# Kernel tuning notes

Hardware: AMD Instinct MI355X
Metric: run time of the kernel (lower is better)

## Reference

```python
import jax, jax.numpy as jnp
import numpy as np

NEG_SLOPE = 0.2  # PyG GATConv default negative_slope
EPS = 1e-16     # PyG softmax denominator epsilon


def gat_conv(x, src, dst, W, a_src, a_dst, bias):
    """PyG GATConv (concat=True, dropout off). x:[N,Fin], src/dst:[E]."""
    N = x.shape[0]
    H, C = a_src.shape
    h = (x @ W).reshape(N, H, C)                      # per-head projected features
    es = jnp.einsum('nhc,hc->nh', h, a_src)           # alpha_src per node/head
    ed = jnp.einsum('nhc,hc->nh', h, a_dst)           # alpha_dst per node/head
    e = jax.nn.leaky_relu(es[src] + ed[dst], NEG_SLOPE)   # [E,H] edge scores
    # segment softmax over destination nodes (every node has a self loop)
    m = jax.ops.segment_max(e, dst, num_segments=N)
    p = jnp.exp(e - m[dst])
    denom = jax.ops.segment_sum(p, dst, num_segments=N)
    alpha = p / (denom[dst] + EPS)                    # [E,H]
    out = jax.ops.segment_sum(h[src] * alpha[:, :, None], dst, num_segments=N)
    return out.reshape(N, H * C) + bias


def _single_graph(x, ei, W1, a_src1, a_dst1, b1, W2, a_src2, a_dst2, b2):
    N = x.shape[0]
    loop = jnp.arange(N, dtype=ei.dtype)              # add_self_loops=True
    src = jnp.concatenate([ei[0], loop])
    dst = jnp.concatenate([ei[1], loop])
    h = jax.nn.relu(gat_conv(x, src, dst, W1, a_src1, a_dst1, b1))
    # F.dropout with p=0.0 is identity
    return gat_conv(h, src, dst, W2, a_src2, a_dst2, b2)


def setup_inputs() -> dict:
    key = jax.random.key(0)
    ks = jax.random.split(key, 9)
    B, N, E, F_in, H, C = 2, 20000, 320000, 128, 8, 64

    def glorot(k, shape):
        fan_in, fan_out = shape[-2] if len(shape) > 1 else shape[-1], shape[-1]
        s = np.sqrt(6.0 / (fan_in + fan_out)).astype(np.float32)
        return jax.random.uniform(k, shape, jnp.float32, -s, s)

    return {
        'xs': jax.random.normal(ks[0], (B, N, F_in), jnp.float32),
        'edge_indexs': jax.random.randint(ks[1], (B, 2, E), 0, N, jnp.int32),
        'W1': glorot(ks[2], (F_in, H * C)),
        'a_src1': glorot(ks[3], (H, C)),
        'a_dst1': glorot(ks[4], (H, C)),
        'b1': jnp.zeros((H * C,), jnp.float32),
        'W2': glorot(ks[5], (H * C, C)),
        'a_src2': glorot(ks[6], (1, C)),
        'a_dst2': glorot(ks[7], (1, C)),
        'b2': jnp.zeros((C,), jnp.float32),
    }


def reference(xs, edge_indexs, W1, a_src1, a_dst1, b1, W2, a_src2, a_dst2, b2):
    f = lambda x, ei: _single_graph(x, ei, W1, a_src1, a_dst1, b1, W2, a_src2, a_dst2, b2)
    return jax.vmap(f)(xs, edge_indexs)               # [B, N, C]
```

## Files before the change

kernel.cpp:

```cpp
#include <hip/hip_runtime.h>
#include <hip/hip_bf16.h>
#include <cstdint>

#define NEG_SLOPE 0.2f
#define SOFTMAX_EPS 1e-16f
#define NN 20000
#define EE 320000
#define CAP 48

typedef __hip_bfloat16 bf16;
typedef unsigned short ushort;
typedef short s8v __attribute__((ext_vector_type(8)));
typedef float f4v __attribute__((ext_vector_type(4)));
typedef float f2v __attribute__((ext_vector_type(2)));

static __device__ __forceinline__ float lo16(unsigned u) { return __uint_as_float(u << 16); }
static __device__ __forceinline__ float hi16(unsigned u) { return __uint_as_float(u & 0xffff0000u); }
static __device__ __forceinline__ ushort f2bf(float v) {
    bf16 h = __float2bfloat16(v);
    return *(ushort*)&h;
}

__global__ void prep_kernel(const float* __restrict__ W1, const float* __restrict__ W2,
                            ushort* __restrict__ w1hi, ushort* __restrict__ w1lo,
                            ushort* __restrict__ w2hi, ushort* __restrict__ w2lo,
                            int* __restrict__ count) {
    int bid = blockIdx.x;
    int t = threadIdx.x;
    if (bid >= 48) {
        int idx = (bid - 48) * 256 + t;
        if (idx < 2 * NN) count[idx] = 0;
        return;
    }
    __shared__ float T[32][65];
    const float* src; ushort *dhi, *dlo; int K, C, c0, k0;
    if (bid < 32) { src = W1; dhi = w1hi; dlo = w1lo; K = 128; C = 512; c0 = (bid & 7) * 64; k0 = (bid >> 3) * 32; }
    else          { src = W2; dhi = w2hi; dlo = w2lo; K = 512; C = 64;  c0 = 0;              k0 = (bid - 32) * 32; }
    for (int i = 0; i < 8; ++i) {
        int flat = t + i * 256;
        int k = flat >> 6, c = flat & 63;
        T[k][c] = src[(size_t)(k0 + k) * C + c0 + c];
    }
    __syncthreads();
    int c = t >> 2, j0 = (t & 3) * 8;
    unsigned hp[4], lp[4];
#pragma unroll
    for (int p = 0; p < 4; ++p) {
        float v0 = T[j0 + p * 2][c], v1 = T[j0 + p * 2 + 1][c];
        ushort h0 = f2bf(v0), h1 = f2bf(v1);
        float l0 = v0 - __uint_as_float((unsigned)h0 << 16);
        float l1 = v1 - __uint_as_float((unsigned)h1 << 16);
        hp[p] = (unsigned)h0 | ((unsigned)h1 << 16);
        lp[p] = (unsigned)f2bf(l0) | ((unsigned)f2bf(l1) << 16);
    }
    size_t o = (size_t)(c0 + c) * K + k0 + j0;
    *(uint4*)&dhi[o] = make_uint4(hp[0], hp[1], hp[2], hp[3]);
    *(uint4*)&dlo[o] = make_uint4(lp[0], lp[1], lp[2], lp[3]);
}

#define G1S 40
#define GEMM1_BLOCKS 1252
__global__ __launch_bounds__(256) void gemm1_scatter(
        const float* __restrict__ xs, const ushort* __restrict__ w1hi,
        const ushort* __restrict__ w1lo, const float* __restrict__ a_src,
        const float* __restrict__ a_dst, bf16* __restrict__ h1,
        float* __restrict__ es, float* __restrict__ ed,
        const int* __restrict__ ei, int* __restrict__ count,
        ushort* __restrict__ esrc) {
    __shared__ ushort lds[25600];
    int t = threadIdx.x;
    int bid = blockIdx.x;

    if (bid >= GEMM1_BLOCKS) {
        int idx = bid - GEMM1_BLOCKS;
        int b = idx / 1250;
        int e = (idx % 1250) * 256 + t;
        const int* srcA = ei + (size_t)b * 2 * EE;
        int s = srcA[e], d = srcA[EE + e];
        if ((unsigned)d >= NN || (unsigned)s >= NN) return;
        int pos = atomicAdd(&count[b * NN + d], 1);
        if (pos < CAP)
            esrc[((size_t)b * NN + d) * CAP + pos] = (ushort)s;
        return;
    }

    ushort* Xhi = lds;
    ushort* Xlo = lds + 2560;
    ushort* Whi = lds + 5120;
    ushort* Wlo = lds + 15360;
    int w = t >> 6, lane = t & 63, quad = lane >> 4, l16 = lane & 15;
    int b = bid / 626;
    int rem = bid % 626;
    int nhalf = rem / 313;
    int row0 = (rem % 313) * 64, nbase = nhalf * 256;
    const float* x = xs + (size_t)b * NN * 128;
    bf16*  h1b = h1 + (size_t)b * NN * 512;
    float* esb = es + (size_t)b * NN * 8;
    float* edb = ed + (size_t)b * NN * 8;

    f4v acc[16];
#pragma unroll
    for (int i = 0; i < 16; ++i) acc[i] = (f4v)0.f;

    for (int kc = 0; kc < 4; ++kc) {
        __syncthreads();
        {
            int row = t >> 2, c0 = (t & 3) * 8;
            float v[8];
            if (row0 + row < NN) {
                float4 A = *(const float4*)&x[(size_t)(row0 + row) * 128 + kc * 32 + c0];
                float4 B = *(const float4*)&x[(size_t)(row0 + row) * 128 + kc * 32 + c0 + 4];
                v[0] = A.x; v[1] = A.y; v[2] = A.z; v[3] = A.w;
                v[4] = B.x; v[5] = B.y; v[6] = B.z; v[7] = B.w;
            } else {
#pragma unroll
                for (int i = 0; i < 8; ++i) v[i] = 0.f;
            }
            unsigned hp[4], lp[4];
#pragma unroll
            for (int p = 0; p < 4; ++p) {
                ushort h0 = f2bf(v[p * 2]), h1_ = f2bf(v[p * 2 + 1]);
                float l0 = v[p * 2] - __uint_as_float((unsigned)h0 << 16);
                float l1 = v[p * 2 + 1] - __uint_as_float((unsigned)h1_ << 16);
                hp[p] = (unsigned)h0 | ((unsigned)h1_ << 16);
                lp[p] = (unsigned)f2bf(l0) | ((unsigned)f2bf(l1) << 16);
            }
            *(uint4*)&Xhi[row * G1S + c0] = make_uint4(hp[0], hp[1], hp[2], hp[3]);
            *(uint4*)&Xlo[row * G1S + c0] = make_uint4(lp[0], lp[1], lp[2], lp[3]);
        }
        {
            const ushort* sh = w1hi + (size_t)(nbase + t) * 128 + kc * 32;
            const ushort* sl = w1lo + (size_t)(nbase + t) * 128 + kc * 32;
            uint4 h0 = *(const uint4*)(sh), h1_ = *(const uint4*)(sh + 8);
            uint4 h2 = *(const uint4*)(sh + 16), h3 = *(const uint4*)(sh + 24);
            uint4 l0 = *(const uint4*)(sl), l1 = *(const uint4*)(sl + 8);
            uint4 l2 = *(const uint4*)(sl + 16), l3 = *(const uint4*)(sl + 24);
            *(uint4*)&Whi[t * G1S]      = h0; *(uint4*)&Whi[t * G1S + 8]  = h1_;
            *(uint4*)&Whi[t * G1S + 16] = h2; *(uint4*)&Whi[t * G1S + 24] = h3;
            *(uint4*)&Wlo[t * G1S]      = l0; *(uint4*)&Wlo[t * G1S + 8]  = l1;
            *(uint4*)&Wlo[t * G1S + 16] = l2; *(uint4*)&Wlo[t * G1S + 24] = l3;
        }
        __syncthreads();
        int arow = (w * 16 + l16) * G1S + quad * 8;
        s8v ahi = *(const s8v*)&Xhi[arow];
        s8v alo = *(const s8v*)&Xlo[arow];
#pragma unroll
        for (int ct = 0; ct < 16; ++ct) {
            int baddr = (ct * 16 + l16) * G1S + quad * 8;
            s8v bhi = *(const s8v*)&Whi[baddr];
            s8v blo = *(const s8v*)&Wlo[baddr];
            acc[ct] = __builtin_amdgcn_mfma_f32_16x16x32_bf16(ahi, bhi, acc[ct], 0, 0, 0);
            acc[ct] = __builtin_amdgcn_mfma_f32_16x16x32_bf16(ahi, blo, acc[ct], 0, 0, 0);
            acc[ct] = __builtin_amdgcn_mfma_f32_16x16x32_bf16(alo, bhi, acc[ct], 0, 0, 0);
        }
    }

#pragma unroll
    for (int hh = 0; hh < 4; ++hh) {
        float s4[4] = {0.f, 0.f, 0.f, 0.f}, d4[4] = {0.f, 0.f, 0.f, 0.f};
#pragma unroll
        for (int ct4 = 0; ct4 < 4; ++ct4) {
            int ct = hh * 4 + ct4;
            int c = nbase + ct * 16 + l16;
            float as = a_src[c], ad = a_dst[c];
#pragma unroll
            for (int r = 0; r < 4; ++r) { s4[r] += acc[ct][r] * as; d4[r] += acc[ct][r] * ad; }
        }
#pragma unroll
        for (int o = 1; o < 16; o <<= 1) {
#pragma unroll
            for (int r = 0; r < 4; ++r) {
                s4[r] += __shfl_xor(s4[r], o);
                d4[r] += __shfl_xor(d4[r], o);
            }
        }
        if (l16 == 0) {
            int head = nhalf * 4 + hh;
#pragma unroll
            for (int r = 0; r < 4; ++r) {
                int gr = row0 + w * 16 + quad * 4 + r;
                if (gr < NN) { esb[gr * 8 + head] = s4[r]; edb[gr * 8 + head] = d4[r]; }
            }
        }
    }

    __syncthreads();
    ushort* rp = lds + w * 4224;
#pragma unroll
    for (int ct = 0; ct < 16; ++ct)
#pragma unroll
        for (int r = 0; r < 4; ++r)
            rp[(quad * 4 + r) * 264 + ct * 16 + l16] = f2bf(acc[ct][r]);
#pragma unroll
    for (int i = 0; i < 8; ++i) {
        int idx = i * 512 + lane * 8;
        int row = idx >> 8, col = idx & 255;
        uint4 vv = *(const uint4*)&rp[row * 264 + col];
        int gr = row0 + w * 16 + row;
        if (gr < NN) *(uint4*)&h1b[(size_t)gr * 512 + nbase + col] = vv;
    }
}

#define G2S 72
__global__ __launch_bounds__(256) void gemm2_mfma(
        const bf16* __restrict__ a, const ushort* __restrict__ w2hi,
        const ushort* __restrict__ w2lo, const float* __restrict__ a_src,
        const float* __restrict__ a_dst, bf16* __restrict__ h2,
        float* __restrict__ es, float* __restrict__ ed) {
    __shared__ ushort lds[13824];
    ushort* AS  = lds;
    ushort* Whi = lds + 4608;
    ushort* Wlo = lds + 9216;

    int t = threadIdx.x;
    int w = t >> 6, lane = t & 63, quad = lane >> 4, l16 = lane & 15;
    int b = blockIdx.y;
    int row0 = blockIdx.x * 64;
    const bf16* ab = a + (size_t)b * NN * 512;
    bf16*  h2b = h2 + (size_t)b * NN * 64;
    float* esb = es + (size_t)b * NN;
    float* edb = ed + (size_t)b * NN;

    f4v acc[4];
#pragma unroll
    for (int i = 0; i < 4; ++i) acc[i] = (f4v)0.f;

    for (int kc = 0; kc < 8; ++kc) {
        __syncthreads();
        {
            int row = t >> 2, k0 = (t & 3) * 16;
            uint4 q0, q1;
            if (row0 + row < NN) {
                q0 = *(const uint4*)(ab + (size_t)(row0 + row) * 512 + kc * 64 + k0);
                q1 = *(const uint4*)(ab + (size_t)(row0 + row) * 512 + kc * 64 + k0 + 8);
            } else { q0 = make_uint4(0, 0, 0, 0); q1 = q0; }
            *(uint4*)&AS[row * G2S + k0]     = q0;
            *(uint4*)&AS[row * G2S + k0 + 8] = q1;
            const ushort* sh = w2hi + (size_t)row * 512 + kc * 64 + k0;
            const ushort* sl = w2lo + (size_t)row * 512 + kc * 64 + k0;
            *(uint4*)&Whi[row * G2S + k0]     = *(const uint4*)(sh);
            *(uint4*)&Whi[row * G2S + k0 + 8] = *(const uint4*)(sh + 8);
            *(uint4*)&Wlo[row * G2S + k0]     = *(const uint4*)(sl);
            *(uint4*)&Wlo[row * G2S + k0 + 8] = *(const uint4*)(sl + 8);
        }
        __syncthreads();
#pragma unroll
        for (int ks = 0; ks < 2; ++ks) {
            s8v av = *(const s8v*)&AS[(w * 16 + l16) * G2S + ks * 32 + quad * 8];
#pragma unroll
            for (int ct = 0; ct < 4; ++ct) {
                int baddr = (ct * 16 + l16) * G2S + ks * 32 + quad * 8;
                s8v bhi = *(const s8v*)&Whi[baddr];
                s8v blo = *(const s8v*)&Wlo[baddr];
                acc[ct] = __builtin_amdgcn_mfma_f32_16x16x32_bf16(av, bhi, acc[ct], 0, 0, 0);
                acc[ct] = __builtin_amdgcn_mfma_f32_16x16x32_bf16(av, blo, acc[ct], 0, 0, 0);
            }
        }
    }

    {
        float s4[4] = {0.f, 0.f, 0.f, 0.f}, d4[4] = {0.f, 0.f, 0.f, 0.f};
#pragma unroll
        for (int ct = 0; ct < 4; ++ct) {
            int c = ct * 16 + l16;
            float as = a_src[c], ad = a_dst[c];
#pragma unroll
            for (int r = 0; r < 4; ++r) { s4[r] += acc[ct][r] * as; d4[r] += acc[ct][r] * ad; }
        }
#pragma unroll
        for (int o = 1; o < 16; o <<= 1) {
#pragma unroll
            for (int r = 0; r < 4; ++r) {
                s4[r] += __shfl_xor(s4[r], o);
                d4[r] += __shfl_xor(d4[r], o);
            }
        }
        if (l16 == 0) {
#pragma unroll
            for (int r = 0; r < 4; ++r) {
                int gr = row0 + w * 16 + quad * 4 + r;
                if (gr < NN) { esb[gr] = s4[r]; edb[gr] = d4[r]; }
            }
        }
    }

    __syncthreads();
    ushort* rp = lds + w * 1152;
#pragma unroll
    for (int ct = 0; ct < 4; ++ct)
#pragma unroll
        for (int r = 0; r < 4; ++r)
            rp[(quad * 4 + r) * G2S + ct * 16 + l16] = f2bf(acc[ct][r]);
#pragma unroll
    for (int i = 0; i < 2; ++i) {
        int idx = i * 512 + lane * 8;
        int row = idx >> 6, col = idx & 63;
        uint4 vv = *(const uint4*)&rp[row * G2S + col];
        int gr = row0 + w * 16 + row;
        if (gr < NN) *(uint4*)&h2b[(size_t)gr * 64 + col] = vv;
    }
}

__global__ __launch_bounds__(256) void aggregate1_kernel(
        const bf16* __restrict__ h1, const float* __restrict__ es,
        const float* __restrict__ ed, const int* __restrict__ count,
        const ushort* __restrict__ esrc, const float* __restrict__ b1,
        bf16* __restrict__ out1) {
    __shared__ float alds[4][8][60];
    __shared__ unsigned offs[4][60];
    int b = blockIdx.y;
    const bf16*  h1b = h1 + (size_t)b * NN * 512;
    const float* esb = es + (size_t)b * NN * 8;
    const float* edb = ed + (size_t)b * NN * 8;
    bf16* out1b = out1 + (size_t)b * NN * 512;

    int t = threadIdx.x;
    int wv = t >> 6, lane = t & 63;
    int n = blockIdx.x * 4 + wv;
    int deg_e = count[b * NN + n];
    deg_e = max(0, min(deg_e, CAP));
    int deg = deg_e + 1;
    size_t beg = ((size_t)b * NN + n) * CAP;

    float4 ed0 = *(const float4*)&edb[n * 8];
    float4 ed1 = *(const float4*)&edb[n * 8 + 4];
    float edh[8] = {ed0.x, ed0.y, ed0.z, ed0.w, ed1.x, ed1.y, ed1.z, ed1.w};

    bool act = lane < deg;
    int sreg = act ? ((lane < deg_e) ? (int)esrc[beg + lane] : n) : 0;
    const char* eb = (const char*)esb;
    unsigned eoff = (unsigned)sreg << 5;
    float4 s0 = *(const float4*)(eb + eoff);
    float4 s1 = *(const float4*)(eb + eoff + 16);
    float e[8] = {s0.x, s0.y, s0.z, s0.w, s1.x, s1.y, s1.z, s1.w};
    float m[8], p[8], sum[8];
#pragma unroll
    for (int h = 0; h < 8; ++h) {
        float v = e[h] + edh[h];
        v = (v >= 0.f) ? v : NEG_SLOPE * v;
        e[h] = act ? v : -1e30f;
        m[h] = e[h];
    }
#pragma unroll
    for (int o = 32; o > 0; o >>= 1) {
#pragma unroll
        for (int h = 0; h < 8; ++h) m[h] = fmaxf(m[h], __shfl_xor(m[h], o));
    }
#pragma unroll
    for (int h = 0; h < 8; ++h) { p[h] = act ? __expf(e[h] - m[h]) : 0.f; sum[h] = p[h]; }
#pragma unroll
    for (int o = 32; o > 0; o >>= 1) {
#pragma unroll
        for (int h = 0; h < 8; ++h) sum[h] += __shfl_xor(sum[h], o);
    }
    if (lane < 60) {
        offs[wv][lane] = act ? ((unsigned)sreg << 10) : 0u;
#pragma unroll
        for (int h = 0; h < 8; ++h)
            alds[wv][h][lane] = p[h] / (sum[h] + SOFTMAX_EPS);
    }

    int mh = lane >> 3;
    unsigned l16b = (unsigned)lane * 16u;
    const bf16* hb = h1b;
    int trips = (deg + 3) >> 2;
    int trips2 = (trips + 1) & ~1;

    f2v acc0 = {0.f, 0.f}, acc1 = {0.f, 0.f}, acc2 = {0.f, 0.f}, acc3 = {0.f, 0.f};
    uint4 A0, A1, A2, A3, B0, B1, B2, B3;
    float4 wA, wB;

#define GLOAD(dst, voff) \
    asm volatile("global_load_dwordx4 %0, %1, %2" : "=&v"(dst) : "v"(voff), "s"(hb))

#define LOADBANK(U0, U1, U2, U3, W4, blk) do { \
        int s_ = (blk) << 2; \
        uint4 ov_ = *(const uint4*)&offs[wv][s_]; \
        W4 = *(const float4*)&alds[wv][mh][s_]; \
        unsigned va_ = ov_.x + l16b, vb_ = ov_.y + l16b; \
        unsigned vc_ = ov_.z + l16b, vd_ = ov_.w + l16b; \
        GLOAD(U0, va_); GLOAD(U1, vb_); GLOAD(U2, vc_); GLOAD(U3, vd_); \
    } while (0)

#define WAITSB(nlit) do { \
        asm volatile("s_waitcnt vmcnt(" #nlit ")" ::: "memory"); \
        __builtin_amdgcn_sched_barrier(0); \
    } while (0)

#define ROW(U, W) do { \
        f2v wp_ = {W, W}; \
        f2v t0_ = {lo16(U.x), hi16(U.x)}; acc0 += t0_ * wp_; \
        f2v t1_ = {lo16(U.y), hi16(U.y)}; acc1 += t1_ * wp_; \
        f2v t2_ = {lo16(U.z), hi16(U.z)}; acc2 += t2_ * wp_; \
        f2v t3_ = {lo16(U.w), hi16(U.w)}; acc3 += t3_ * wp_; \
    } while (0)

#define CONSUME(U0, U1, U2, U3, W4) do { \
        ROW(U0, W4.x); ROW(U1, W4.y); ROW(U2, W4.z); ROW(U3, W4.w); \
    } while (0)

    LOADBANK(A0, A1, A2, A3, wA, 0);
    LOADBANK(B0, B1, B2, B3, wB, 1);
    for (int it = 0; it + 2 < trips2; it += 2) {
        WAITSB(4);
        CONSUME(A0, A1, A2, A3, wA); LOADBANK(A0, A1, A2, A3, wA, it + 2);
        WAITSB(4);
        CONSUME(B0, B1, B2, B3, wB); LOADBANK(B0, B1, B2, B3, wB, it + 3);
    }
    WAITSB(4);
    CONSUME(A0, A1, A2, A3, wA);
    WAITSB(0);
    CONSUME(B0, B1, B2, B3, wB);

#undef GLOAD
#undef LOADBANK
#undef WAITSB
#undef ROW
#undef CONSUME

    float accs[8] = {acc0.x, acc0.y, acc1.x, acc1.y, acc2.x, acc2.y, acc3.x, acc3.y};
    float4 bv0 = *(const float4*)&b1[lane * 8];
    float4 bv1 = *(const float4*)&b1[lane * 8 + 4];
    float bias[8] = {bv0.x, bv0.y, bv0.z, bv0.w, bv1.x, bv1.y, bv1.z, bv1.w};
    union { ushort us[8]; uint4 u4; } pack;
#pragma unroll
    for (int i = 0; i < 8; ++i)
        pack.us[i] = f2bf(fmaxf(accs[i] + bias[i], 0.f));
    *(uint4*)(out1b + (size_t)n * 512 + lane * 8) = pack.u4;
}

__global__ void aggregate2_kernel(const bf16* __restrict__ h2, const float* __restrict__ es,
                                  const float* __restrict__ ed, const int* __restrict__ count,
                                  const ushort* __restrict__ esrc, const float* __restrict__ bias2,
                                  float* __restrict__ out) {
    __shared__ float wl[4][64];
    __shared__ int slidx[4][64];
    int b = blockIdx.y;
    const bf16*  h2b = h2 + (size_t)b * NN * 64;
    const float* esb = es + (size_t)b * NN;
    const float* edb = ed + (size_t)b * NN;
    float* outb = out + (size_t)b * NN * 64;

    int t = threadIdx.x;
    int wv = t >> 6, lane = t & 63;
    int n = blockIdx.x * 4 + wv;
    int deg_e = count[b * NN + n];
    deg_e = max(0, min(deg_e, CAP));
    int deg = deg_e + 1;
    size_t beg = ((size_t)b * NN + n) * CAP;
    float edn = edb[n];

    bool act = lane < deg;
    int sreg = act ? ((lane < deg_e) ? (int)esrc[beg + lane] : n) : 0;
    float ev = act ? esb[sreg] + edn : -1e30f;
    ev = (ev >= 0.f) ? ev : NEG_SLOPE * ev;
    if (!act) ev = -1e30f;
    float m = ev;
#pragma unroll
    for (int o = 32; o > 0; o >>= 1) m = fmaxf(m, __shfl_xor(m, o));
    float p = act ? __expf(ev - m) : 0.f;
    float sum = p;
#pragma unroll
    for (int o = 32; o > 0; o >>= 1) sum += __shfl_xor(sum, o);
    slidx[wv][lane] = sreg;
    wl[wv][lane] = p / (sum + SOFTMAX_EPS);

    float acc[4] = {0.f, 0.f, 0.f, 0.f};
    int grp = lane >> 4, ch4 = (lane & 15) * 4;
    int j = grp;
    for (; j + 4 < deg; j += 8) {
        int sA = slidx[wv][j];     float wA = wl[wv][j];
        int sB = slidx[wv][j + 4]; float wB = wl[wv][j + 4];
        uint2 uA = *(const uint2*)(h2b + (size_t)sA * 64 + ch4);
        uint2 uB = *(const uint2*)(h2b + (size_t)sB * 64 + ch4);
        acc[0] += wA * lo16(uA.x); acc[1] += wA * hi16(uA.x);
        acc[2] += wA * lo16(uA.y); acc[3] += wA * hi16(uA.y);
        acc[0] += wB * lo16(uB.x); acc[1] += wB * hi16(uB.x);
        acc[2] += wB * lo16(uB.y); acc[3] += wB * hi16(uB.y);
    }
    for (; j < deg; j += 4) {
        int s = slidx[wv][j];
        float wt = wl[wv][j];
        uint2 u = *(const uint2*)(h2b + (size_t)s * 64 + ch4);
        acc[0] += wt * lo16(u.x); acc[1] += wt * hi16(u.x);
        acc[2] += wt * lo16(u.y); acc[3] += wt * hi16(u.y);
    }
#pragma unroll
    for (int i = 0; i < 4; ++i) {
        acc[i] += __shfl_xor(acc[i], 16);
        acc[i] += __shfl_xor(acc[i], 32);
    }
    if (lane < 16) {
        float4 o4;
        o4.x = acc[0] + bias2[ch4 + 0];
        o4.y = acc[1] + bias2[ch4 + 1];
        o4.z = acc[2] + bias2[ch4 + 2];
        o4.w = acc[3] + bias2[ch4 + 3];
        *(float4*)&outb[(size_t)n * 64 + ch4] = o4;
    }
}

extern "C" void kernel_launch(void* const* d_in, const int* in_sizes, int n_in,
                              void* d_out, int out_size, void* d_ws, size_t ws_size,
                              hipStream_t stream) {
    const float* xs     = (const float*)d_in[0];
    const int*   ei     = (const int*)d_in[1];
    const float* W1     = (const float*)d_in[2];
    const float* a_src1 = (const float*)d_in[3];
    const float* a_dst1 = (const float*)d_in[4];
    const float* b1     = (const float*)d_in[5];
    const float* W2     = (const float*)d_in[6];
    const float* a_src2 = (const float*)d_in[7];
    const float* a_dst2 = (const float*)d_in[8];
    const float* b2     = (const float*)d_in[9];
    float* out = (float*)d_out;

    const int B = 2;

    uintptr_t p = (uintptr_t)d_ws;
    auto alloc = [&](size_t bytes) {
        void* r = (void*)p;
        p += (bytes + 255) & ~(size_t)255;
        return r;
    };
    bf16* h1   = (bf16*)alloc((size_t)B * NN * 512 * 2);
    bf16* out1 = (bf16*)alloc((size_t)B * NN * 512 * 2);
    char* unionA = (char*)alloc((size_t)B * NN * 64 * 2);
    float*  es1   = (float*)unionA;
    float*  ed1   = (float*)(unionA + 1280000);
    ushort* wt1hi = (ushort*)(unionA + 2560000);
    ushort* wt1lo = (ushort*)(unionA + 2560000 + 131072);
    bf16*   h2    = (bf16*)unionA;
    ushort* wt2hi = (ushort*)alloc((size_t)64 * 512 * 2);
    ushort* wt2lo = (ushort*)alloc((size_t)64 * 512 * 2);
    float* es2    = (float*)alloc((size_t)B * NN * 4);
    float* ed2    = (float*)alloc((size_t)B * NN * 4);
    int*   count  = (int*)alloc((size_t)B * NN * 4);
    ushort* esrc  = (ushort*)alloc((size_t)B * NN * CAP * 2);

    const int initBlocks = (2 * NN + 255) / 256;
    prep_kernel<<<48 + initBlocks, 256, 0, stream>>>(W1, W2, wt1hi, wt1lo, wt2hi, wt2lo, count);
    gemm1_scatter<<<GEMM1_BLOCKS + 2500, 256, 0, stream>>>(xs, wt1hi, wt1lo, a_src1, a_dst1,
                                                           h1, es1, ed1, ei, count, esrc);
    aggregate1_kernel<<<dim3(NN / 4, B), 256, 0, stream>>>(h1, es1, ed1, count, esrc, b1, out1);
    gemm2_mfma<<<dim3(313, B), 256, 0, stream>>>(out1, wt2hi, wt2lo, a_src2, a_dst2, h2, es2, ed2);
    aggregate2_kernel<<<dim3(NN / 4, B), 256, 0, stream>>>(h2, es2, ed2, count, esrc, b2, out);
}
```

Measured before the change: 271.0 us.

## Remap aggregation blocks to XCDs and split layer-1 heads into halves

Both aggregation kernels now use a 1D grid and derive batch and node range from the block index modulo 8. Each XCD then handles a contiguous slice of one graph, so that graph's gathered features stay in that XCD's L2. Layer-1 aggregation additionally splits the 8 heads into two halves per block, doubling the block count. Each wave gathers 8-byte instead of 16-byte chunks, which cuts register pressure and narrows each XCD's working set. The cost is smaller, less efficient gather loads, and the edge-score softmax is now computed twice per node.

```diff
diff --git a/kernel.cpp b/kernel.cpp
--- a/kernel.cpp
+++ b/kernel.cpp
@@ -306,36 +306,41 @@
         const float* __restrict__ ed, const int* __restrict__ count,
         const ushort* __restrict__ esrc, const float* __restrict__ b1,
         bf16* __restrict__ out1) {
-    __shared__ float alds[4][8][60];
+    __shared__ float alds[4][4][60];
     __shared__ unsigned offs[4][60];
-    int b = blockIdx.y;
+
+    int t = threadIdx.x;
+    int wv = t >> 6, lane = t & 63;
+    int bid = blockIdx.x;
+    int xcd = bid & 7;
+    int q = bid >> 3;
+    int combo = xcd >> 1;
+    int b = combo >> 1;
+    int half = combo & 1;
+    int n = (xcd & 1) * 10000 + q * 4 + wv;
+
     const bf16*  h1b = h1 + (size_t)b * NN * 512;
     const float* esb = es + (size_t)b * NN * 8;
     const float* edb = ed + (size_t)b * NN * 8;
     bf16* out1b = out1 + (size_t)b * NN * 512;
 
-    int t = threadIdx.x;
-    int wv = t >> 6, lane = t & 63;
-    int n = blockIdx.x * 4 + wv;
     int deg_e = count[b * NN + n];
     deg_e = max(0, min(deg_e, CAP));
     int deg = deg_e + 1;
     size_t beg = ((size_t)b * NN + n) * CAP;
 
-    float4 ed0 = *(const float4*)&edb[n * 8];
-    float4 ed1 = *(const float4*)&edb[n * 8 + 4];
-    float edh[8] = {ed0.x, ed0.y, ed0.z, ed0.w, ed1.x, ed1.y, ed1.z, ed1.w};
+    float4 edv = *(const float4*)&edb[n * 8 + half * 4];
+    float edh[4] = {edv.x, edv.y, edv.z, edv.w};
 
     bool act = lane < deg;
     int sreg = act ? ((lane < deg_e) ? (int)esrc[beg + lane] : n) : 0;
     const char* eb = (const char*)esb;
-    unsigned eoff = (unsigned)sreg << 5;
+    unsigned eoff = ((unsigned)sreg << 5) + (unsigned)half * 16u;
     float4 s0 = *(const float4*)(eb + eoff);
-    float4 s1 = *(const float4*)(eb + eoff + 16);
-    float e[8] = {s0.x, s0.y, s0.z, s0.w, s1.x, s1.y, s1.z, s1.w};
-    float m[8], p[8], sum[8];
-#pragma unroll
-    for (int h = 0; h < 8; ++h) {
+    float e[4] = {s0.x, s0.y, s0.z, s0.w};
+    float m[4], p[4], sum[4];
+#pragma unroll
+    for (int h = 0; h < 4; ++h) {
         float v = e[h] + edh[h];
         v = (v >= 0.f) ? v : NEG_SLOPE * v;
         e[h] = act ? v : -1e30f;
@@ -344,41 +349,41 @@
 #pragma unroll
     for (int o = 32; o > 0; o >>= 1) {
 #pragma unroll
-        for (int h = 0; h < 8; ++h) m[h] = fmaxf(m[h], __shfl_xor(m[h], o));
-    }
-#pragma unroll
-    for (int h = 0; h < 8; ++h) { p[h] = act ? __expf(e[h] - m[h]) : 0.f; sum[h] = p[h]; }
+        for (int h = 0; h < 4; ++h) m[h] = fmaxf(m[h], __shfl_xor(m[h], o));
+    }
+#pragma unroll
+    for (int h = 0; h < 4; ++h) { p[h] = act ? __expf(e[h] - m[h]) : 0.f; sum[h] = p[h]; }
 #pragma unroll
     for (int o = 32; o > 0; o >>= 1) {
 #pragma unroll
-        for (int h = 0; h < 8; ++h) sum[h] += __shfl_xor(sum[h], o);
+        for (int h = 0; h < 4; ++h) sum[h] += __shfl_xor(sum[h], o);
     }
     if (lane < 60) {
         offs[wv][lane] = act ? ((unsigned)sreg << 10) : 0u;
 #pragma unroll
-        for (int h = 0; h < 8; ++h)
+        for (int h = 0; h < 4; ++h)
             alds[wv][h][lane] = p[h] / (sum[h] + SOFTMAX_EPS);
     }
 
-    int mh = lane >> 3;
-    unsigned l16b = (unsigned)lane * 16u;
+    int mh = lane >> 4;
+    unsigned l8b = (unsigned)half * 512u + (unsigned)lane * 8u;
     const bf16* hb = h1b;
     int trips = (deg + 3) >> 2;
     int trips2 = (trips + 1) & ~1;
 
-    f2v acc0 = {0.f, 0.f}, acc1 = {0.f, 0.f}, acc2 = {0.f, 0.f}, acc3 = {0.f, 0.f};
-    uint4 A0, A1, A2, A3, B0, B1, B2, B3;
+    f2v acc0 = {0.f, 0.f}, acc1 = {0.f, 0.f};
+    uint2 A0, A1, A2, A3, B0, B1, B2, B3;
     float4 wA, wB;
 
 #define GLOAD(dst, voff) \
-    asm volatile("global_load_dwordx4 %0, %1, %2" : "=&v"(dst) : "v"(voff), "s"(hb))
+    asm volatile("global_load_dwordx2 %0, %1, %2" : "=&v"(dst) : "v"(voff), "s"(hb))
 
 #define LOADBANK(U0, U1, U2, U3, W4, blk) do { \
         int s_ = (blk) << 2; \
         uint4 ov_ = *(const uint4*)&offs[wv][s_]; \
         W4 = *(const float4*)&alds[wv][mh][s_]; \
-        unsigned va_ = ov_.x + l16b, vb_ = ov_.y + l16b; \
-        unsigned vc_ = ov_.z + l16b, vd_ = ov_.w + l16b; \
+        unsigned va_ = ov_.x + l8b, vb_ = ov_.y + l8b; \
+        unsigned vc_ = ov_.z + l8b, vd_ = ov_.w + l8b; \
         GLOAD(U0, va_); GLOAD(U1, vb_); GLOAD(U2, vc_); GLOAD(U3, vd_); \
     } while (0)
 
@@ -391,8 +396,6 @@
         f2v wp_ = {W, W}; \
         f2v t0_ = {lo16(U.x), hi16(U.x)}; acc0 += t0_ * wp_; \
         f2v t1_ = {lo16(U.y), hi16(U.y)}; acc1 += t1_ * wp_; \
-        f2v t2_ = {lo16(U.z), hi16(U.z)}; acc2 += t2_ * wp_; \
-        f2v t3_ = {lo16(U.w), hi16(U.w)}; acc3 += t3_ * wp_; \
     } while (0)
 
 #define CONSUME(U0, U1, U2, U3, W4) do { \
@@ -418,15 +421,14 @@
 #undef ROW
 #undef CONSUME
 
-    float accs[8] = {acc0.x, acc0.y, acc1.x, acc1.y, acc2.x, acc2.y, acc3.x, acc3.y};
-    float4 bv0 = *(const float4*)&b1[lane * 8];
-    float4 bv1 = *(const float4*)&b1[lane * 8 + 4];
-    float bias[8] = {bv0.x, bv0.y, bv0.z, bv0.w, bv1.x, bv1.y, bv1.z, bv1.w};
-    union { ushort us[8]; uint4 u4; } pack;
-#pragma unroll
-    for (int i = 0; i < 8; ++i)
+    float accs[4] = {acc0.x, acc0.y, acc1.x, acc1.y};
+    float4 bv = *(const float4*)&b1[half * 256 + lane * 4];
+    float bias[4] = {bv.x, bv.y, bv.z, bv.w};
+    union { ushort us[4]; uint2 u2; } pack;
+#pragma unroll
+    for (int i = 0; i < 4; ++i)
         pack.us[i] = f2bf(fmaxf(accs[i] + bias[i], 0.f));
-    *(uint4*)(out1b + (size_t)n * 512 + lane * 8) = pack.u4;
+    *(uint2*)(out1b + (size_t)n * 512 + half * 256 + lane * 4) = pack.u2;
 }
 
 __global__ void aggregate2_kernel(const bf16* __restrict__ h2, const float* __restrict__ es,
@@ -435,15 +437,19 @@
                                   float* __restrict__ out) {
     __shared__ float wl[4][64];
     __shared__ int slidx[4][64];
-    int b = blockIdx.y;
+    int t = threadIdx.x;
+    int wv = t >> 6, lane = t & 63;
+    int bid = blockIdx.x;
+    int xcd = bid & 7;
+    int q = bid >> 3;
+    int b = xcd >> 2;
+    int n = (xcd & 3) * 5000 + q * 4 + wv;
+
     const bf16*  h2b = h2 + (size_t)b * NN * 64;
     const float* esb = es + (size_t)b * NN;
     const float* edb = ed + (size_t)b * NN;
     float* outb = out + (size_t)b * NN * 64;
 
-    int t = threadIdx.x;
-    int wv = t >> 6, lane = t & 63;
-    int n = blockIdx.x * 4 + wv;
     int deg_e = count[b * NN + n];
     deg_e = max(0, min(deg_e, CAP));
     int deg = deg_e + 1;
@@ -542,7 +548,7 @@
     prep_kernel<<<48 + initBlocks, 256, 0, stream>>>(W1, W2, wt1hi, wt1lo, wt2hi, wt2lo, count);
     gemm1_scatter<<<GEMM1_BLOCKS + 2500, 256, 0, stream>>>(xs, wt1hi, wt1lo, a_src1, a_dst1,
                                                            h1, es1, ed1, ei, count, esrc);
-    aggregate1_kernel<<<dim3(NN / 4, B), 256, 0, stream>>>(h1, es1, ed1, count, esrc, b1, out1);
+    aggregate1_kernel<<<20000, 256, 0, stream>>>(h1, es1, ed1, count, esrc, b1, out1);
     gemm2_mfma<<<dim3(313, B), 256, 0, stream>>>(out1, wt2hi, wt2lo, a_src2, a_dst2, h2, es2, ed2);
-    aggregate2_kernel<<<dim3(NN / 4, B), 256, 0, stream>>>(h2, es2, ed2, count, esrc, b2, out);
-}
+    aggregate2_kernel<<<10000, 256, 0, stream>>>(h2, es2, ed2, count, esrc, b2, out);
+}
```

Result: faster. 261.6 us (-3.5%).
